# Performance work log

Measured on AMD Instinct MI355X. Metric: run time of the kernel, lower is better.

The kernel has to match this reference:

```python
import jax, jax.numpy as jnp
import numpy as np

HEADS = 16
DIM_HEAD = 64
DIM = 1024
EPS = 1e-5


def _layernorm(x, g, b):
    mu = jnp.mean(x, axis=-1, keepdims=True)
    var = jnp.var(x, axis=-1, keepdims=True)
    return (x - mu) * jax.lax.rsqrt(var + EPS) * g + b


def setup_inputs() -> dict:
    key = jax.random.key(0)
    ks = jax.random.split(key, 8)
    inner = HEADS * DIM_HEAD  # 1024
    x = jax.random.normal(ks[0], (2, 2048, DIM), dtype=jnp.float32)
    w_qkv = jax.random.normal(ks[1], (DIM, inner * 3), dtype=jnp.float32) * (DIM ** -0.5)
    w_out = jax.random.normal(ks[2], (inner, DIM), dtype=jnp.float32) * (inner ** -0.5)
    ln1_g = jnp.ones((DIM,), jnp.float32)
    ln1_b = jnp.zeros((DIM,), jnp.float32)
    ln2_g = jnp.ones((DIM,), jnp.float32)
    ln2_b = jnp.zeros((DIM,), jnp.float32)
    return {"x": x, "ln1_g": ln1_g, "ln1_b": ln1_b, "w_qkv": w_qkv,
            "w_out": w_out, "ln2_g": ln2_g, "ln2_b": ln2_b}


def reference(x, ln1_g, ln1_b, w_qkv, w_out, ln2_g, ln2_b):
    b, n, _ = x.shape
    scale = DIM_HEAD ** -0.5
    xn = _layernorm(x, ln1_g, ln1_b)
    qkv = xn @ w_qkv  # [b, n, 3*inner]
    q, k, v = jnp.split(qkv, 3, axis=-1)
    # b n (h d) -> b h n d
    resh = lambda t: t.reshape(b, n, HEADS, DIM_HEAD).transpose(0, 2, 1, 3)
    q, k, v = resh(q) * scale, resh(k), resh(v)
    sim = jnp.einsum('bhid,bhjd->bhij', q, k)
    causal = jnp.tril(jnp.ones((n, n), dtype=bool))
    # masked_fill(triu(1), 0) followed by relu == relu masked to lower triangle
    attn = jnp.where(causal, jax.nn.relu(sim), 0.0)
    out = jnp.einsum('bhij,bhjd->bhid', attn, v)
    out = out.transpose(0, 2, 1, 3).reshape(b, n, HEADS * DIM_HEAD)
    return _layernorm(out @ w_out, ln2_g, ln2_b)
```

## Files before the change

kernel.cpp:

```cpp
#include <hip/hip_runtime.h>
#include <cstdint>
#include <cstddef>


typedef __bf16 bf16_t;
typedef __bf16 bf16x8 __attribute__((ext_vector_type(8)));
typedef __bf16 bf16x4 __attribute__((ext_vector_type(4)));
typedef float  f32x4  __attribute__((ext_vector_type(4)));

#define DEV_INLINE __device__ __forceinline__

DEV_INLINE void async_copy16(void* lds, const void* g) {
  __builtin_amdgcn_global_load_lds(
      (__attribute__((address_space(1))) void*)(g),
      (__attribute__((address_space(3))) void*)(lds), 16, 0, 0);
}

__global__ __launch_bounds__(256) void ln1_kernel(
    const float* __restrict__ x, const float* __restrict__ g,
    const float* __restrict__ bta, bf16_t* __restrict__ xn) {
  const int row = blockIdx.x;
  const int t = threadIdx.x, w = t >> 6, l = t & 63;
  const float* xr = x + (size_t)row * 1024;
  float4 v = *(const float4*)(xr + t * 4);
  float s  = v.x + v.y + v.z + v.w;
  float s2 = v.x * v.x + v.y * v.y + v.z * v.z + v.w * v.w;
  #pragma unroll
  for (int off = 32; off >= 1; off >>= 1) {
    s  += __shfl_down(s, off);
    s2 += __shfl_down(s2, off);
  }
  __shared__ float red[8];
  if (l == 0) { red[w] = s; red[4 + w] = s2; }
  __syncthreads();
  s  = red[0] + red[1] + red[2] + red[3];
  s2 = red[4] + red[5] + red[6] + red[7];
  float mu  = s * (1.0f / 1024.0f);
  float var = s2 * (1.0f / 1024.0f) - mu * mu;
  float rs  = rsqrtf(var + 1e-5f);
  float4 gv = *(const float4*)(g + t * 4);
  float4 bv = *(const float4*)(bta + t * 4);
  bf16x4 o;
  o[0] = (bf16_t)((v.x - mu) * rs * gv.x + bv.x);
  o[1] = (bf16_t)((v.y - mu) * rs * gv.y + bv.y);
  o[2] = (bf16_t)((v.z - mu) * rs * gv.z + bv.z);
  o[3] = (bf16_t)((v.w - mu) * rs * gv.w + bv.w);
  *(bf16x4*)(xn + (size_t)row * 1024 + t * 4) = o;
}

__global__ __launch_bounds__(256) void ln2_kernel(
    const float* __restrict__ z0, const float* __restrict__ z1,
    const float* __restrict__ g, const float* __restrict__ bta,
    float* __restrict__ out) {
  const int row = blockIdx.x;
  const int t = threadIdx.x, w = t >> 6, l = t & 63;
  float4 v  = *(const float4*)(z0 + (size_t)row * 1024 + t * 4);
  float4 v1 = *(const float4*)(z1 + (size_t)row * 1024 + t * 4);
  v.x += v1.x; v.y += v1.y; v.z += v1.z; v.w += v1.w;
  float s  = v.x + v.y + v.z + v.w;
  float s2 = v.x * v.x + v.y * v.y + v.z * v.z + v.w * v.w;
  #pragma unroll
  for (int off = 32; off >= 1; off >>= 1) {
    s  += __shfl_down(s, off);
    s2 += __shfl_down(s2, off);
  }
  __shared__ float red[8];
  if (l == 0) { red[w] = s; red[4 + w] = s2; }
  __syncthreads();
  s  = red[0] + red[1] + red[2] + red[3];
  s2 = red[4] + red[5] + red[6] + red[7];
  float mu  = s * (1.0f / 1024.0f);
  float var = s2 * (1.0f / 1024.0f) - mu * mu;
  float rs  = rsqrtf(var + 1e-5f);
  float4 gv = *(const float4*)(g + t * 4);
  float4 bv = *(const float4*)(bta + t * 4);
  float4 o;
  o.x = (v.x - mu) * rs * gv.x + bv.x;
  o.y = (v.y - mu) * rs * gv.y + bv.y;
  o.z = (v.z - mu) * rs * gv.z + bv.z;
  o.w = (v.w - mu) * rs * gv.w + bv.w;
  *(float4*)(out + (size_t)row * 1024 + t * 4) = o;
}

__global__ __launch_bounds__(256) void wtrans_kernel(
    const float* __restrict__ wsrc, bf16_t* __restrict__ wdstT, int N) {
  __shared__ __align__(16) float tl[64][68];
  const int n0 = blockIdx.x * 64, k0 = blockIdx.y * 64;
  const int t = threadIdx.x;
  #pragma unroll
  for (int c = 0; c < 4; ++c) {
    int idx = c * 256 + t;
    int r = idx >> 4, c4 = (idx & 15) * 4;
    *(float4*)&tl[r][c4] = *(const float4*)(wsrc + (size_t)(k0 + r) * N + n0 + c4);
  }
  __syncthreads();
  #pragma unroll
  for (int c = 0; c < 2; ++c) {
    int idx = c * 256 + t;
    int nl = idx >> 3, kc = (idx & 7) * 8;
    bf16x8 o;
    #pragma unroll
    for (int ii = 0; ii < 8; ++ii) o[ii] = (bf16_t)tl[kc + ii][nl];
    *(bf16x8*)(wdstT + (size_t)(n0 + nl) * 1024 + k0 + kc) = o;
  }
}

__global__ __launch_bounds__(256) void vtrans_kernel(
    const bf16_t* __restrict__ v, bf16_t* __restrict__ vT) {
  __shared__ __align__(16) bf16_t tl[64][72];
  const int n0 = blockIdx.x * 64;
  const size_t bh = blockIdx.y;
  const int t = threadIdx.x;
  #pragma unroll
  for (int c = 0; c < 2; ++c) {
    int idx = c * 256 + t;
    int r = idx >> 3, c8 = (idx & 7) * 8;
    *(bf16x8*)&tl[r][c8] = *(const bf16x8*)(v + (bh * 2048 + n0 + r) * 64 + c8);
  }
  __syncthreads();
  #pragma unroll
  for (int c = 0; c < 2; ++c) {
    int idx = c * 256 + t;
    int d = idx >> 3, nc = (idx & 7) * 8;
    bf16x8 o;
    #pragma unroll
    for (int ii = 0; ii < 8; ++ii) o[ii] = tl[nc + ii][d];
    *(bf16x8*)(vT + (bh * 64 + d) * 2048 + n0 + nc) = o;
  }
}

template <int EPI, int KSPLIT>
__global__ __launch_bounds__(256, 3) void gemm128_kernel(
    const bf16_t* __restrict__ A, const bf16_t* __restrict__ Bt,
    void* __restrict__ C0, void* __restrict__ C1, void* __restrict__ C2) {
  __shared__ __align__(16) bf16_t As[128 * 32];
  __shared__ __align__(16) bf16_t Bs[128 * 32];
  const int t = threadIdx.x;
  const int w = t >> 6, l = t & 63, l15 = l & 15, quad = l >> 4;
  const int wy = w >> 1, wx = w & 1;
  const int m0 = blockIdx.y * 128, n0 = blockIdx.x * 128;
  const int kz = (KSPLIT > 1) ? blockIdx.z : 0;
  const int kt0 = kz * (32 / KSPLIT), kt1 = kt0 + (32 / KSPLIT);

  int arow[2], acol[2];
  #pragma unroll
  for (int c = 0; c < 2; ++c) {
    int e = (w * 2 + c) * 512 + l * 8;
    arow[c] = e >> 5;
    acol[c] = e & 31;
  }

  f32x4 acc[4][4];
  #pragma unroll
  for (int i = 0; i < 4; ++i)
    #pragma unroll
    for (int j = 0; j < 4; ++j) acc[i][j] = (f32x4)0.0f;

  for (int kt = kt0; kt < kt1; ++kt) {
    __syncthreads();
    #pragma unroll
    for (int c = 0; c < 2; ++c) {
      async_copy16(&As[(w * 2 + c) * 512],
                   A + (size_t)(m0 + arow[c]) * 1024 + kt * 32 + acol[c]);
      async_copy16(&Bs[(w * 2 + c) * 512],
                   Bt + (size_t)(n0 + arow[c]) * 1024 + kt * 32 + acol[c]);
    }
    __syncthreads();
    bf16x8 af[4], bfr[4];
    #pragma unroll
    for (int i = 0; i < 4; ++i)
      af[i] = *(const bf16x8*)&As[(wy * 64 + i * 16 + l15) * 32 + quad * 8];
    #pragma unroll
    for (int j = 0; j < 4; ++j)
      bfr[j] = *(const bf16x8*)&Bs[(wx * 64 + j * 16 + l15) * 32 + quad * 8];
    #pragma unroll
    for (int i = 0; i < 4; ++i)
      #pragma unroll
      for (int j = 0; j < 4; ++j)
        acc[i][j] = __builtin_amdgcn_mfma_f32_16x16x32_bf16(af[i], bfr[j], acc[i][j], 0, 0, 0);
  }

  if (EPI == 0) {
    float* C = (float*)(kz == 0 ? C0 : C1);
    #pragma unroll
    for (int i = 0; i < 4; ++i)
      #pragma unroll
      for (int j = 0; j < 4; ++j)
        #pragma unroll
        for (int r = 0; r < 4; ++r) {
          int m = m0 + wy * 64 + i * 16 + quad * 4 + r;
          int n = n0 + wx * 64 + j * 16 + l15;
          C[(size_t)m * 1024 + n] = acc[i][j][r];
        }
  } else {
    int nb = n0 + wx * 64;
    int which = nb >> 10;
    int head = (nb & 1023) >> 6;
    bf16_t* dst = which == 0 ? (bf16_t*)C0 : which == 1 ? (bf16_t*)C1 : (bf16_t*)C2;
    float sc = which == 0 ? 0.125f : 1.0f;
    #pragma unroll
    for (int i = 0; i < 4; ++i)
      #pragma unroll
      for (int j = 0; j < 4; ++j)
        #pragma unroll
        for (int r = 0; r < 4; ++r) {
          int m = m0 + wy * 64 + i * 16 + quad * 4 + r;
          int bq = m >> 11, pos = m & 2047;
          int d = j * 16 + l15;
          dst[(((size_t)(bq * 16 + head)) * 2048 + pos) * 64 + d] =
              (bf16_t)(acc[i][j][r] * sc);
        }
  }
}

__global__ __launch_bounds__(256, 2) void attn_kernel(
    const bf16_t* __restrict__ q, const bf16_t* __restrict__ k,
    const bf16_t* __restrict__ vT, bf16_t* __restrict__ out) {
  __shared__ __align__(16) bf16_t Ks[2][128 * 64];
  __shared__ __align__(16) bf16_t Vts[2][128 * 64];
  __shared__ __align__(16) bf16_t Ss[64 * 72];

  const int h = blockIdx.x, p = blockIdx.y, b = blockIdx.z;
  const int t = threadIdx.x;
  const int w = t >> 6, l = t & 63, l15 = l & 15, quad = l >> 4;
  const size_t bh = (size_t)(b * 16 + h);
  const int tB = 31 - p;

  const int r_l = l >> 3;
  const int u_g = (l & 7) ^ r_l;
  const int rswz = l15 & 7;

  auto stage_tile = [&](int buf, int half, int kt2) {
    #pragma unroll
    for (int c = 0; c < 2; ++c) {
      int idx = w * 2 + c;
      int row = idx * 8 + r_l;
      async_copy16(&Ks[buf][half * 4096 + idx * 512],
                   k + (bh * 2048 + kt2 * 64 + row) * 64 + u_g * 8);
      async_copy16(&Vts[buf][half * 4096 + idx * 512],
                   vT + (bh * 64 + row) * 2048 + kt2 * 64 + u_g * 8);
    }
  };
  auto stage_it = [&](int it, int buf) {
    if (it <= p) {
      stage_tile(buf, 0, it);
    } else {
      int base = p + 1 + 2 * (it - p - 1);
      stage_tile(buf, 0, base);
      int k2 = base + 1; if (k2 > 31) k2 = 31;
      stage_tile(buf, 1, k2);
    }
  };

  bf16x8 qa[2][2];
  {
    int rA = p * 64 + w * 16, rB = tB * 64 + w * 16;
    #pragma unroll
    for (int kk = 0; kk < 2; ++kk) {
      qa[0][kk] = *(const bf16x8*)(q + (bh * 2048 + rA + l15) * 64 + kk * 32 + quad * 8);
      qa[1][kk] = *(const bf16x8*)(q + (bh * 2048 + rB + l15) * 64 + kk * 32 + quad * 8);
    }
  }

  f32x4 acc0[4], acc1[4];
  #pragma unroll
  for (int tj = 0; tj < 4; ++tj) { acc0[tj] = (f32x4)0.0f; acc1[tj] = (f32x4)0.0f; }

  auto unit = [&](f32x4 (&accr)[4], bf16x8 (&qf)[2],
                  const bf16_t* Kb, const bf16_t* Vb, bool dg) {
    f32x4 sacc[4];
    #pragma unroll
    for (int tj = 0; tj < 4; ++tj) sacc[tj] = (f32x4)0.0f;
    #pragma unroll
    for (int kk = 0; kk < 2; ++kk)
      #pragma unroll
      for (int tj = 0; tj < 4; ++tj) {
        bf16x8 bk = *(const bf16x8*)&Kb[(tj * 16 + l15) * 64 + (((kk * 4 + quad) ^ rswz) * 8)];
        sacc[tj] = __builtin_amdgcn_mfma_f32_16x16x32_bf16(qf[kk], bk, sacc[tj], 0, 0, 0);
      }
    #pragma unroll
    for (int tj = 0; tj < 4; ++tj)
      #pragma unroll
      for (int r = 0; r < 4; ++r) {
        float v = fmaxf(sacc[tj][r], 0.0f);
        if (dg && (tj * 16 + l15 > w * 16 + quad * 4 + r)) v = 0.0f;
        Ss[(w * 16 + quad * 4 + r) * 72 + tj * 16 + l15] = (bf16_t)v;
      }
    #pragma unroll
    for (int kk = 0; kk < 2; ++kk) {
      bf16x8 as_ = *(const bf16x8*)&Ss[(w * 16 + l15) * 72 + kk * 32 + quad * 8];
      #pragma unroll
      for (int tj = 0; tj < 4; ++tj) {
        bf16x8 bv = *(const bf16x8*)&Vb[(tj * 16 + l15) * 64 + (((kk * 4 + quad) ^ rswz) * 8)];
        accr[tj] = __builtin_amdgcn_mfma_f32_16x16x32_bf16(as_, bv, accr[tj], 0, 0, 0);
      }
    }
  };

  stage_it(0, 0);
  for (int it = 0; it < 17; ++it) {
    __syncthreads();
    if (it + 1 < 17) stage_it(it + 1, (it + 1) & 1);
    const int buf = it & 1;
    if (it <= p) {
      unit(acc0, qa[0], &Ks[buf][0], &Vts[buf][0], it == p);
      unit(acc1, qa[1], &Ks[buf][0], &Vts[buf][0], false);
    } else {
      int base = p + 1 + 2 * (it - p - 1);
      unit(acc1, qa[1], &Ks[buf][0], &Vts[buf][0], base == tB);
      if (base + 1 <= tB)
        unit(acc1, qa[1], &Ks[buf][4096], &Vts[buf][4096], base + 1 == tB);
    }
  }

  #pragma unroll
  for (int tj = 0; tj < 4; ++tj)
    #pragma unroll
    for (int r = 0; r < 4; ++r) {
      int col = h * 64 + tj * 16 + l15;
      int posA = p * 64 + w * 16 + quad * 4 + r;
      int posB = tB * 64 + w * 16 + quad * 4 + r;
      out[((size_t)b * 2048 + posA) * 1024 + col] = (bf16_t)acc0[tj][r];
      out[((size_t)b * 2048 + posB) * 1024 + col] = (bf16_t)acc1[tj][r];
    }
}

extern "C" void kernel_launch(void* const* d_in, const int* in_sizes, int n_in,
                              void* d_out, int out_size, void* d_ws, size_t ws_size,
                              hipStream_t stream) {
  (void)in_sizes; (void)n_in; (void)out_size; (void)ws_size;
  const float* x     = (const float*)d_in[0];
  const float* ln1_g = (const float*)d_in[1];
  const float* ln1_b = (const float*)d_in[2];
  const float* w_qkv = (const float*)d_in[3];
  const float* w_out = (const float*)d_in[4];
  const float* ln2_g = (const float*)d_in[5];
  const float* ln2_b = (const float*)d_in[6];
  float* out = (float*)d_out;

  char* ws = (char*)d_ws;
  bf16_t* xn     = (bf16_t*)(ws + 0);
  bf16_t* wqkvT  = (bf16_t*)(ws + 8388608);
  bf16_t* woutT  = (bf16_t*)(ws + 14680064);
  bf16_t* qb     = (bf16_t*)(ws + 16777216);
  bf16_t* kb     = (bf16_t*)(ws + 25165824);
  bf16_t* vb     = (bf16_t*)(ws + 33554432);
  bf16_t* vTb    = (bf16_t*)(ws + 41943040);
  bf16_t* ao     = (bf16_t*)(ws + 50331648);
  float*  z0     = (float*)(ws + 58720256);
  float*  z1     = (float*)(ws + 16777216);

  ln1_kernel<<<4096, 256, 0, stream>>>(x, ln1_g, ln1_b, xn);
  wtrans_kernel<<<dim3(48, 16), 256, 0, stream>>>(w_qkv, wqkvT, 3072);
  wtrans_kernel<<<dim3(16, 16), 256, 0, stream>>>(w_out, woutT, 1024);
  gemm128_kernel<1, 1><<<dim3(24, 32), 256, 0, stream>>>(xn, wqkvT, qb, kb, vb);
  vtrans_kernel<<<dim3(32, 32), 256, 0, stream>>>(vb, vTb);
  attn_kernel<<<dim3(16, 16, 2), 256, 0, stream>>>(qb, kb, vTb, ao);
  gemm128_kernel<0, 2><<<dim3(8, 32, 2), 256, 0, stream>>>(ao, woutT, z0, z1, nullptr);
  ln2_kernel<<<4096, 256, 0, stream>>>(z0, z1, ln2_g, ln2_b, out);
}
```

Before: 194.1 us.

## Halve attention LDS staging and load second tile directly to registers

Cuts the attention kernel's double-buffered K/V LDS tiles from two 64-row halves to one. In the tail phase the second tile is now read straight from global memory into registers instead of through LDS. Fragments are loaded once into registers and shared by both units in the diagonal phase, and launch bounds are raised to 3 blocks per SM. The goal is higher occupancy and less LDS traffic. The cost is uncoalesced-ish direct global loads with no async prefetch, plus more register pressure under the tighter bound.

```diff
diff --git a/kernel.cpp b/kernel.cpp
--- a/kernel.cpp
+++ b/kernel.cpp
@@ -213,11 +213,11 @@
   }
 }
 
-__global__ __launch_bounds__(256, 2) void attn_kernel(
+__global__ __launch_bounds__(256, 3) void attn_kernel(
     const bf16_t* __restrict__ q, const bf16_t* __restrict__ k,
     const bf16_t* __restrict__ vT, bf16_t* __restrict__ out) {
-  __shared__ __align__(16) bf16_t Ks[2][128 * 64];
-  __shared__ __align__(16) bf16_t Vts[2][128 * 64];
+  __shared__ __align__(16) bf16_t Ks[2][64 * 64];
+  __shared__ __align__(16) bf16_t Vts[2][64 * 64];
   __shared__ __align__(16) bf16_t Ss[64 * 72];
 
   const int h = blockIdx.x, p = blockIdx.y, b = blockIdx.z;
@@ -230,26 +230,43 @@
   const int u_g = (l & 7) ^ r_l;
   const int rswz = l15 & 7;
 
-  auto stage_tile = [&](int buf, int half, int kt2) {
+  auto stage_tile = [&](int buf, int kt2) {
     #pragma unroll
     for (int c = 0; c < 2; ++c) {
       int idx = w * 2 + c;
       int row = idx * 8 + r_l;
-      async_copy16(&Ks[buf][half * 4096 + idx * 512],
+      async_copy16(&Ks[buf][idx * 512],
                    k + (bh * 2048 + kt2 * 64 + row) * 64 + u_g * 8);
-      async_copy16(&Vts[buf][half * 4096 + idx * 512],
+      async_copy16(&Vts[buf][idx * 512],
                    vT + (bh * 64 + row) * 2048 + kt2 * 64 + u_g * 8);
     }
   };
   auto stage_it = [&](int it, int buf) {
-    if (it <= p) {
-      stage_tile(buf, 0, it);
-    } else {
-      int base = p + 1 + 2 * (it - p - 1);
-      stage_tile(buf, 0, base);
-      int k2 = base + 1; if (k2 > 31) k2 = 31;
-      stage_tile(buf, 1, k2);
-    }
+    int kt2 = (it <= p) ? it : (p + 1 + 2 * (it - p - 1));
+    stage_tile(buf, kt2);
+  };
+
+  auto load_lds = [&](const bf16_t* Kb, const bf16_t* Vb,
+                      bf16x8 (&bk)[2][4], bf16x8 (&bv)[2][4]) {
+    #pragma unroll
+    for (int kk = 0; kk < 2; ++kk)
+      #pragma unroll
+      for (int tj = 0; tj < 4; ++tj) {
+        int u = ((kk * 4 + quad) ^ rswz) * 8;
+        bk[kk][tj] = *(const bf16x8*)&Kb[(tj * 16 + l15) * 64 + u];
+        bv[kk][tj] = *(const bf16x8*)&Vb[(tj * 16 + l15) * 64 + u];
+      }
+  };
+  auto load_global = [&](int kt2, bf16x8 (&bk)[2][4], bf16x8 (&bv)[2][4]) {
+    #pragma unroll
+    for (int kk = 0; kk < 2; ++kk)
+      #pragma unroll
+      for (int tj = 0; tj < 4; ++tj) {
+        bk[kk][tj] = *(const bf16x8*)(k  + (bh * 2048 + kt2 * 64 + tj * 16 + l15) * 64
+                                         + kk * 32 + quad * 8);
+        bv[kk][tj] = *(const bf16x8*)(vT + (bh * 64 + tj * 16 + l15) * 2048
+                                         + kt2 * 64 + kk * 32 + quad * 8);
+      }
   };
 
   bf16x8 qa[2][2];
@@ -267,17 +284,15 @@
   for (int tj = 0; tj < 4; ++tj) { acc0[tj] = (f32x4)0.0f; acc1[tj] = (f32x4)0.0f; }
 
   auto unit = [&](f32x4 (&accr)[4], bf16x8 (&qf)[2],
-                  const bf16_t* Kb, const bf16_t* Vb, bool dg) {
+                  bf16x8 (&bk)[2][4], bf16x8 (&bv)[2][4], bool dg) {
     f32x4 sacc[4];
     #pragma unroll
     for (int tj = 0; tj < 4; ++tj) sacc[tj] = (f32x4)0.0f;
     #pragma unroll
     for (int kk = 0; kk < 2; ++kk)
       #pragma unroll
-      for (int tj = 0; tj < 4; ++tj) {
-        bf16x8 bk = *(const bf16x8*)&Kb[(tj * 16 + l15) * 64 + (((kk * 4 + quad) ^ rswz) * 8)];
-        sacc[tj] = __builtin_amdgcn_mfma_f32_16x16x32_bf16(qf[kk], bk, sacc[tj], 0, 0, 0);
-      }
+      for (int tj = 0; tj < 4; ++tj)
+        sacc[tj] = __builtin_amdgcn_mfma_f32_16x16x32_bf16(qf[kk], bk[kk][tj], sacc[tj], 0, 0, 0);
     #pragma unroll
     for (int tj = 0; tj < 4; ++tj)
       #pragma unroll
@@ -290,10 +305,8 @@
     for (int kk = 0; kk < 2; ++kk) {
       bf16x8 as_ = *(const bf16x8*)&Ss[(w * 16 + l15) * 72 + kk * 32 + quad * 8];
       #pragma unroll
-      for (int tj = 0; tj < 4; ++tj) {
-        bf16x8 bv = *(const bf16x8*)&Vb[(tj * 16 + l15) * 64 + (((kk * 4 + quad) ^ rswz) * 8)];
-        accr[tj] = __builtin_amdgcn_mfma_f32_16x16x32_bf16(as_, bv, accr[tj], 0, 0, 0);
-      }
+      for (int tj = 0; tj < 4; ++tj)
+        accr[tj] = __builtin_amdgcn_mfma_f32_16x16x32_bf16(as_, bv[kk][tj], accr[tj], 0, 0, 0);
     }
   };
 
@@ -303,13 +316,19 @@
     if (it + 1 < 17) stage_it(it + 1, (it + 1) & 1);
     const int buf = it & 1;
     if (it <= p) {
-      unit(acc0, qa[0], &Ks[buf][0], &Vts[buf][0], it == p);
-      unit(acc1, qa[1], &Ks[buf][0], &Vts[buf][0], false);
+      bf16x8 bk[2][4], bv[2][4];
+      load_lds(&Ks[buf][0], &Vts[buf][0], bk, bv);
+      unit(acc0, qa[0], bk, bv, it == p);
+      unit(acc1, qa[1], bk, bv, false);
     } else {
       int base = p + 1 + 2 * (it - p - 1);
-      unit(acc1, qa[1], &Ks[buf][0], &Vts[buf][0], base == tB);
-      if (base + 1 <= tB)
-        unit(acc1, qa[1], &Ks[buf][4096], &Vts[buf][4096], base + 1 == tB);
+      bool second = (base + 1 <= tB);
+      bf16x8 bk2[2][4], bv2[2][4];
+      if (second) load_global(base + 1, bk2, bv2);
+      bf16x8 bk[2][4], bv[2][4];
+      load_lds(&Ks[buf][0], &Vts[buf][0], bk, bv);
+      unit(acc1, qa[1], bk, bv, base == tB);
+      if (second) unit(acc1, qa[1], bk2, bv2, base + 1 == tB);
     }
   }
 
```

Result: slower. 311.4 us (+60.4%).

## Double GEMM K-tile to 64 with XOR-swizzled LDS; hoist attention K/V fragments

Applied to the files above, without the earlier changes.

The GEMM kernel now stages 64-wide K tiles instead of 32, using an XOR swizzle on the LDS layout to avoid bank conflicts. This halves the number of barrier-separated load iterations and gives each sync two MFMA k-steps. The attention kernel preloads the K and V fragments from LDS into registers once per tile and shares them between the two query blocks, removing duplicate LDS reads. The cost is higher register use and doubled LDS per GEMM block, which may reduce occupancy under launch_bounds(256,3).

```diff
diff --git a/kernel.cpp b/kernel.cpp
--- a/kernel.cpp
+++ b/kernel.cpp
@@ -133,22 +133,18 @@
 __global__ __launch_bounds__(256, 3) void gemm128_kernel(
     const bf16_t* __restrict__ A, const bf16_t* __restrict__ Bt,
     void* __restrict__ C0, void* __restrict__ C1, void* __restrict__ C2) {
-  __shared__ __align__(16) bf16_t As[128 * 32];
-  __shared__ __align__(16) bf16_t Bs[128 * 32];
+  __shared__ __align__(16) bf16_t As[128 * 64];
+  __shared__ __align__(16) bf16_t Bs[128 * 64];
   const int t = threadIdx.x;
   const int w = t >> 6, l = t & 63, l15 = l & 15, quad = l >> 4;
   const int wy = w >> 1, wx = w & 1;
   const int m0 = blockIdx.y * 128, n0 = blockIdx.x * 128;
   const int kz = (KSPLIT > 1) ? blockIdx.z : 0;
-  const int kt0 = kz * (32 / KSPLIT), kt1 = kt0 + (32 / KSPLIT);
-
-  int arow[2], acol[2];
-  #pragma unroll
-  for (int c = 0; c < 2; ++c) {
-    int e = (w * 2 + c) * 512 + l * 8;
-    arow[c] = e >> 5;
-    acol[c] = e & 31;
-  }
+  const int kt0 = kz * (16 / KSPLIT), kt1 = kt0 + (16 / KSPLIT);
+
+  const int r_l = l >> 3;
+  const int u_src = (l & 7) ^ r_l;
+  const int rswz = l15 & 7;
 
   f32x4 acc[4][4];
   #pragma unroll
@@ -159,25 +155,28 @@
   for (int kt = kt0; kt < kt1; ++kt) {
     __syncthreads();
     #pragma unroll
-    for (int c = 0; c < 2; ++c) {
-      async_copy16(&As[(w * 2 + c) * 512],
-                   A + (size_t)(m0 + arow[c]) * 1024 + kt * 32 + acol[c]);
-      async_copy16(&Bs[(w * 2 + c) * 512],
-                   Bt + (size_t)(n0 + arow[c]) * 1024 + kt * 32 + acol[c]);
+    for (int c = 0; c < 4; ++c) {
+      int idx = w * 4 + c;
+      int row = idx * 8 + r_l;
+      async_copy16(&As[idx * 512], A + (size_t)(m0 + row) * 1024 + kt * 64 + u_src * 8);
+      async_copy16(&Bs[idx * 512], Bt + (size_t)(n0 + row) * 1024 + kt * 64 + u_src * 8);
     }
     __syncthreads();
-    bf16x8 af[4], bfr[4];
-    #pragma unroll
-    for (int i = 0; i < 4; ++i)
-      af[i] = *(const bf16x8*)&As[(wy * 64 + i * 16 + l15) * 32 + quad * 8];
-    #pragma unroll
-    for (int j = 0; j < 4; ++j)
-      bfr[j] = *(const bf16x8*)&Bs[(wx * 64 + j * 16 + l15) * 32 + quad * 8];
-    #pragma unroll
-    for (int i = 0; i < 4; ++i)
+    #pragma unroll
+    for (int kk = 0; kk < 2; ++kk) {
+      bf16x8 af[4], bfr[4];
+      #pragma unroll
+      for (int i = 0; i < 4; ++i)
+        af[i] = *(const bf16x8*)&As[(wy * 64 + i * 16 + l15) * 64 + (((kk * 4 + quad) ^ rswz) * 8)];
       #pragma unroll
       for (int j = 0; j < 4; ++j)
-        acc[i][j] = __builtin_amdgcn_mfma_f32_16x16x32_bf16(af[i], bfr[j], acc[i][j], 0, 0, 0);
+        bfr[j] = *(const bf16x8*)&Bs[(wx * 64 + j * 16 + l15) * 64 + (((kk * 4 + quad) ^ rswz) * 8)];
+      #pragma unroll
+      for (int i = 0; i < 4; ++i)
+        #pragma unroll
+        for (int j = 0; j < 4; ++j)
+          acc[i][j] = __builtin_amdgcn_mfma_f32_16x16x32_bf16(af[i], bfr[j], acc[i][j], 0, 0, 0);
+    }
   }
 
   if (EPI == 0) {
@@ -252,6 +251,18 @@
     }
   };
 
+  auto load_lds = [&](const bf16_t* Kb, const bf16_t* Vb,
+                      bf16x8 (&bk)[2][4], bf16x8 (&bv)[2][4]) {
+    #pragma unroll
+    for (int kk = 0; kk < 2; ++kk)
+      #pragma unroll
+      for (int tj = 0; tj < 4; ++tj) {
+        int u = ((kk * 4 + quad) ^ rswz) * 8;
+        bk[kk][tj] = *(const bf16x8*)&Kb[(tj * 16 + l15) * 64 + u];
+        bv[kk][tj] = *(const bf16x8*)&Vb[(tj * 16 + l15) * 64 + u];
+      }
+  };
+
   bf16x8 qa[2][2];
   {
     int rA = p * 64 + w * 16, rB = tB * 64 + w * 16;
@@ -267,17 +278,15 @@
   for (int tj = 0; tj < 4; ++tj) { acc0[tj] = (f32x4)0.0f; acc1[tj] = (f32x4)0.0f; }
 
   auto unit = [&](f32x4 (&accr)[4], bf16x8 (&qf)[2],
-                  const bf16_t* Kb, const bf16_t* Vb, bool dg) {
+                  bf16x8 (&bk)[2][4], bf16x8 (&bv)[2][4], bool dg) {
     f32x4 sacc[4];
     #pragma unroll
     for (int tj = 0; tj < 4; ++tj) sacc[tj] = (f32x4)0.0f;
     #pragma unroll
     for (int kk = 0; kk < 2; ++kk)
       #pragma unroll
-      for (int tj = 0; tj < 4; ++tj) {
-        bf16x8 bk = *(const bf16x8*)&Kb[(tj * 16 + l15) * 64 + (((kk * 4 + quad) ^ rswz) * 8)];
-        sacc[tj] = __builtin_amdgcn_mfma_f32_16x16x32_bf16(qf[kk], bk, sacc[tj], 0, 0, 0);
-      }
+      for (int tj = 0; tj < 4; ++tj)
+        sacc[tj] = __builtin_amdgcn_mfma_f32_16x16x32_bf16(qf[kk], bk[kk][tj], sacc[tj], 0, 0, 0);
     #pragma unroll
     for (int tj = 0; tj < 4; ++tj)
       #pragma unroll
@@ -290,10 +299,8 @@
     for (int kk = 0; kk < 2; ++kk) {
       bf16x8 as_ = *(const bf16x8*)&Ss[(w * 16 + l15) * 72 + kk * 32 + quad * 8];
       #pragma unroll
-      for (int tj = 0; tj < 4; ++tj) {
-        bf16x8 bv = *(const bf16x8*)&Vb[(tj * 16 + l15) * 64 + (((kk * 4 + quad) ^ rswz) * 8)];
-        accr[tj] = __builtin_amdgcn_mfma_f32_16x16x32_bf16(as_, bv, accr[tj], 0, 0, 0);
-      }
+      for (int tj = 0; tj < 4; ++tj)
+        accr[tj] = __builtin_amdgcn_mfma_f32_16x16x32_bf16(as_, bv[kk][tj], accr[tj], 0, 0, 0);
     }
   };
 
@@ -302,14 +309,18 @@
     __syncthreads();
     if (it + 1 < 17) stage_it(it + 1, (it + 1) & 1);
     const int buf = it & 1;
+    bf16x8 bk[2][4], bv[2][4];
+    load_lds(&Ks[buf][0], &Vts[buf][0], bk, bv);
     if (it <= p) {
-      unit(acc0, qa[0], &Ks[buf][0], &Vts[buf][0], it == p);
-      unit(acc1, qa[1], &Ks[buf][0], &Vts[buf][0], false);
+      unit(acc0, qa[0], bk, bv, it == p);
+      unit(acc1, qa[1], bk, bv, false);
     } else {
       int base = p + 1 + 2 * (it - p - 1);
-      unit(acc1, qa[1], &Ks[buf][0], &Vts[buf][0], base == tB);
-      if (base + 1 <= tB)
-        unit(acc1, qa[1], &Ks[buf][4096], &Vts[buf][4096], base + 1 == tB);
+      unit(acc1, qa[1], bk, bv, base == tB);
+      if (base + 1 <= tB) {
+        load_lds(&Ks[buf][4096], &Vts[buf][4096], bk, bv);
+        unit(acc1, qa[1], bk, bv, base + 1 == tB);
+      }
     }
   }
 
```

Result: faster. 186.8 us (-3.8%).
